# Performance work log

Measured on AMD Instinct MI355X. Metric: run time of the kernel, lower is better.

Reference implementation:

```python
import jax, jax.numpy as jnp
import numpy as np

HIDDEN = 64
NUM_HEADS = 2
HEAD_DIM = HIDDEN // NUM_HEADS  # 32


def setup_inputs() -> dict:
    key = jax.random.key(0)
    ks = jax.random.split(key, 10)
    B, L = 8, 2048
    s = 1.0 / np.sqrt(HIDDEN)
    return {
        "hidden_states": jax.random.normal(ks[0], (B, L, HIDDEN), dtype=jnp.float32),
        "qx": jax.random.normal(ks[1], (B, L, HIDDEN), dtype=jnp.float32),
        "Wq": jax.random.uniform(ks[2], (HIDDEN, HIDDEN), jnp.float32, -s, s),
        "bq": jax.random.uniform(ks[3], (HIDDEN,), jnp.float32, -s, s),
        "Wk": jax.random.uniform(ks[4], (HIDDEN, HIDDEN), jnp.float32, -s, s),
        "bk": jax.random.uniform(ks[5], (HIDDEN,), jnp.float32, -s, s),
        "Wv": jax.random.uniform(ks[6], (HIDDEN, HIDDEN), jnp.float32, -s, s),
        "bv": jax.random.uniform(ks[7], (HIDDEN,), jnp.float32, -s, s),
        "Wo": jax.random.uniform(ks[8], (HIDDEN, HIDDEN), jnp.float32, -s, s),
        "bo": jax.random.uniform(ks[9], (HIDDEN,), jnp.float32, -s, s),
    }


def _split_heads(x):
    # [B, L, HIDDEN] -> [B, H, L, HEAD_DIM]
    B, L, _ = x.shape
    return x.reshape(B, L, NUM_HEADS, HEAD_DIM).transpose(0, 2, 1, 3)


def reference(hidden_states, qx, Wq, bq, Wk, bk, Wv, bv, Wo, bo):
    # NOTE: faithful to original - query AND value come from qx, key from hidden_states.
    q = _split_heads(qx @ Wq.T + bq)              # [B, H, Lq, D]
    k = _split_heads(hidden_states @ Wk.T + bk)   # [B, H, Lk, D]
    v = _split_heads(qx @ Wv.T + bv)              # [B, H, Lq, D]
    scores = jnp.einsum("bhqd,bhkd->bhqk", q, k) / np.sqrt(HEAD_DIM).astype(np.float32)
    probs = jax.nn.softmax(scores, axis=-1)       # [B, H, Lq, Lk]
    ctx = jnp.einsum("bhqk,bhkd->bhqd", probs, v)
    B, H, L, D = ctx.shape
    ctx = ctx.transpose(0, 2, 1, 3).reshape(B, L, H * D)
    out = ctx @ Wo.T + bo
    return out, probs
```

## Files before the change

### kernel.cpp

```cpp
#include <hip/hip_runtime.h>
#include <math.h>

#define NB 8
#define SEQ 2048
#define HID 64
#define HDIM 32
#define ROWS (NB * SEQ)
#define OUT_ELEMS (ROWS * HID)
#define QSCALE 0.25503486f

typedef __attribute__((ext_vector_type(8))) short bf16x8;
typedef __attribute__((ext_vector_type(4))) float f32x4;
typedef __attribute__((ext_vector_type(4))) uint u32x4;

__device__ __forceinline__ ushort f2bf(float f) {
    uint u = __builtin_bit_cast(uint, f);
    u += 0x7FFFu + ((u >> 16) & 1u);
    return (ushort)(u >> 16);
}
__device__ __forceinline__ float bf2f(ushort h) {
    uint u = ((uint)h) << 16;
    return __builtin_bit_cast(float, u);
}
__device__ __forceinline__ uint cvt_pk_bf16(float lo, float hi) {
    uint r;
    asm("v_cvt_pk_bf16_f32 %0, %1, %2" : "=v"(r) : "v"(lo), "v"(hi));
    return r;
}
__device__ __forceinline__ void glds16(const ushort* g, ushort* l) {
    __builtin_amdgcn_global_load_lds(
        (const __attribute__((address_space(1))) uint*)(g),
        (__attribute__((address_space(3))) uint*)(l), 16, 0, 0);
}

__global__ __launch_bounds__(256, 1)
void qkv_proj_kernel(const float* __restrict__ hs, const float* __restrict__ qx,
                     const float* __restrict__ Wq, const float* __restrict__ bq,
                     const float* __restrict__ Wk, const float* __restrict__ bk,
                     const float* __restrict__ Wv, const float* __restrict__ bv,
                     ushort* __restrict__ q_hi, ushort* __restrict__ q_lo,
                     ushort* __restrict__ k_hi, ushort* __restrict__ vt_hi)
{
    __shared__ __align__(16) float xq_lds[64][64];
    __shared__ __align__(16) float xh_lds[64][64];
    __shared__ float vbuf[64][65];

    const int t  = threadIdx.x;
    const int r0 = blockIdx.x * 64;
    const int b  = r0 >> 11;

#pragma unroll
    for (int u = 0; u < 4; ++u) {
        const int idx = t + 256 * u;
        const int rr = idx >> 4, kk = (idx & 15) * 4;
        *(float4*)&xq_lds[rr][kk] = *(const float4*)(qx + (size_t)(r0 + rr) * HID + kk);
        *(float4*)&xh_lds[rr][kk] = *(const float4*)(hs + (size_t)(r0 + rr) * HID + kk);
    }
    __syncthreads();

    const int c = t & 63, w = t >> 6;
    const int rw = w * 16;
    const int h = c >> 5, d = c & 31;
    const size_t obase = ((size_t)((b * 2 + h) * SEQ) + (r0 & 2047) + rw) * 32 + d;

    {
        float4 wr[16];
#pragma unroll
        for (int i = 0; i < 16; ++i) wr[i] = *(const float4*)(Wq + c * 64 + 4 * i);
        const float bc = bq[c];
        f32x4 acc[16];
#pragma unroll
        for (int r = 0; r < 16; ++r) acc[r] = (f32x4){0.f, 0.f, 0.f, 0.f};
#pragma unroll
        for (int k4 = 0; k4 < 16; ++k4)
#pragma unroll
            for (int r = 0; r < 16; ++r) {
                const float4 x4 = *(const float4*)&xq_lds[rw + r][k4 * 4];
                acc[r][0] += x4.x * wr[k4].x; acc[r][1] += x4.y * wr[k4].y;
                acc[r][2] += x4.z * wr[k4].z; acc[r][3] += x4.w * wr[k4].w;
            }
#pragma unroll
        for (int r = 0; r < 16; ++r) {
            const float v = (acc[r][0] + acc[r][1] + acc[r][2] + acc[r][3] + bc) * QSCALE;
            const ushort hv = f2bf(v);
            q_hi[obase + (size_t)r * 32] = hv;
            q_lo[obase + (size_t)r * 32] = f2bf(v - bf2f(hv));
        }
    }
    {
        float4 wr[16];
#pragma unroll
        for (int i = 0; i < 16; ++i) wr[i] = *(const float4*)(Wk + c * 64 + 4 * i);
        const float bc = bk[c];
        f32x4 acc[16];
#pragma unroll
        for (int r = 0; r < 16; ++r) acc[r] = (f32x4){0.f, 0.f, 0.f, 0.f};
#pragma unroll
        for (int k4 = 0; k4 < 16; ++k4)
#pragma unroll
            for (int r = 0; r < 16; ++r) {
                const float4 x4 = *(const float4*)&xh_lds[rw + r][k4 * 4];
                acc[r][0] += x4.x * wr[k4].x; acc[r][1] += x4.y * wr[k4].y;
                acc[r][2] += x4.z * wr[k4].z; acc[r][3] += x4.w * wr[k4].w;
            }
#pragma unroll
        for (int r = 0; r < 16; ++r) {
            const float v = acc[r][0] + acc[r][1] + acc[r][2] + acc[r][3] + bc;
            k_hi[obase + (size_t)r * 32] = f2bf(v);
        }
    }
    {
        float4 wr[16];
#pragma unroll
        for (int i = 0; i < 16; ++i) wr[i] = *(const float4*)(Wv + c * 64 + 4 * i);
        const float bc = bv[c];
        f32x4 acc[16];
#pragma unroll
        for (int r = 0; r < 16; ++r) acc[r] = (f32x4){0.f, 0.f, 0.f, 0.f};
#pragma unroll
        for (int k4 = 0; k4 < 16; ++k4)
#pragma unroll
            for (int r = 0; r < 16; ++r) {
                const float4 x4 = *(const float4*)&xq_lds[rw + r][k4 * 4];
                acc[r][0] += x4.x * wr[k4].x; acc[r][1] += x4.y * wr[k4].y;
                acc[r][2] += x4.z * wr[k4].z; acc[r][3] += x4.w * wr[k4].w;
            }
#pragma unroll
        for (int r = 0; r < 16; ++r)
            vbuf[rw + r][c] = acc[r][0] + acc[r][1] + acc[r][2] + acc[r][3] + bc;
    }
    __syncthreads();

#pragma unroll
    for (int g = 0; g < 2; ++g) {
        const int row8 = (g * 4 + w) * 8;
        bf16x8 hi8;
#pragma unroll
        for (int e = 0; e < 8; ++e) hi8[e] = (short)f2bf(vbuf[row8 + e][c]);
        const size_t vo = ((size_t)((b * 2 + h) * 32) + d) * SEQ + (r0 & 2047) + row8;
        *reinterpret_cast<bf16x8*>(vt_hi + vo) = hi8;
    }
}

__global__ __launch_bounds__(256, 2)
void zsum_kernel(const ushort* __restrict__ q_hi, const ushort* __restrict__ q_lo,
                 const ushort* __restrict__ k_hi, float* __restrict__ rz_ws)
{
    __shared__ float z_buf[4][64];

    const int bid   = blockIdx.x;
    const int swz   = (bid & 7) * 64 + (bid >> 3);
    const int slice = swz >> 5;
    const int qb    = swz & 31;
    const int q0 = qb * 64;

    const int tid  = threadIdx.x;
    const int w    = tid >> 6, lane = tid & 63;
    const int lg   = lane >> 4, li = lane & 15;
    const int cq0  = w * 512;

    bf16x8 aqh[4], aql[4];
#pragma unroll
    for (int rt = 0; rt < 4; ++rt) {
        const size_t qoff = ((size_t)slice * SEQ + q0 + rt * 16 + li) * 32 + lg * 8;
        aqh[rt] = *(const bf16x8*)(q_hi + qoff);
        aql[rt] = *(const bf16x8*)(q_lo + qoff);
    }
    const size_t kbase = (size_t)slice * SEQ * 32;
    auto Kf = [&](int j16) {
        return *(const bf16x8*)(k_hi + kbase + (size_t)(cq0 + j16 * 16 + li) * 32 + lg * 8);
    };

    float zacc[16];
#pragma unroll
    for (int i = 0; i < 16; ++i) zacc[i] = 0.f;
    bf16x8 bh = Kf(0);
#pragma unroll 2
    for (int ct = 0; ct < 32; ++ct) {
        const bf16x8 bn = Kf(ct < 31 ? ct + 1 : 31);
#pragma unroll
        for (int rt = 0; rt < 4; ++rt) {
            f32x4 a = {0.f, 0.f, 0.f, 0.f};
            a = __builtin_amdgcn_mfma_f32_16x16x32_bf16(aqh[rt], bh, a, 0, 0, 0);
            a = __builtin_amdgcn_mfma_f32_16x16x32_bf16(aql[rt], bh, a, 0, 0, 0);
#pragma unroll
            for (int r = 0; r < 4; ++r) zacc[rt * 4 + r] += __builtin_amdgcn_exp2f(a[r]);
        }
        bh = bn;
    }
#pragma unroll
    for (int m = 1; m < 16; m <<= 1)
#pragma unroll
        for (int i = 0; i < 16; ++i) zacc[i] += __shfl_xor(zacc[i], m, 64);
    if (li == 0) {
#pragma unroll
        for (int rt = 0; rt < 4; ++rt)
#pragma unroll
            for (int r = 0; r < 4; ++r)
                z_buf[w][rt * 16 + lg * 4 + r] = zacc[rt * 4 + r];
    }
    __syncthreads();
    if (tid < 64) {
        const float z = z_buf[0][tid] + z_buf[1][tid] + z_buf[2][tid] + z_buf[3][tid];
        rz_ws[(size_t)slice * SEQ + q0 + tid] = 1.0f / z;
    }
}

__global__ __launch_bounds__(512, 4)
void attn_kernel(const ushort* __restrict__ q_hi, const ushort* __restrict__ q_lo,
                 const ushort* __restrict__ k_hi, const ushort* __restrict__ vt_hi,
                 const float* __restrict__ rz_ws, float* __restrict__ d_out)
{
    __shared__ __align__(16) ushort kbuf[3][2048];
    __shared__ __align__(16) ushort vbuf[3][2048];
    __shared__ __align__(16) float  ps[64 * 68];

    const int bid   = blockIdx.x;
    const int swz   = (bid & 7) * 64 + (bid >> 3);
    const int slice = swz >> 5;
    const int qb    = swz & 31;
    const int bb = slice >> 1, hh = slice & 1;
    const int q0 = qb * 64;

    const int tid  = threadIdx.x;
    const int wid  = tid >> 6, lane = tid & 63;
    const int lg   = lane >> 4, li = lane & 15;
    const int rt   = wid & 3;
    const int cs   = wid >> 2;

    const size_t qoff = ((size_t)slice * SEQ + q0 + rt * 16 + li) * 32 + lg * 8;
    const bf16x8 aqh = *(const bf16x8*)(q_hi + qoff);
    const bf16x8 aql = *(const bf16x8*)(q_lo + qoff);

    float rcpz[4];
#pragma unroll
    for (int r = 0; r < 4; ++r)
        rcpz[r] = rz_ws[(size_t)slice * SEQ + q0 + rt * 16 + lg * 4 + r];

    const ushort* kslice = k_hi + (size_t)slice * SEQ * 32;
    const ushort* vslice = vt_hi + (size_t)slice * 32 * SEQ;
    float* probs = d_out + OUT_ELEMS + ((size_t)slice * SEQ + q0) * SEQ;

    auto STAGE = [&](int t, int ring) {
        const int j0 = t * 64;
        if (wid < 4) {
            const int col = wid * 16 + (lane >> 2);
            const int cg  = (lane & 3) ^ ((lane >> 2) & 3);
            glds16(kslice + (size_t)(j0 + col) * 32 + cg * 8,
                   &kbuf[ring][wid * 512 + lane * 8]);
        } else {
            const int w2  = wid - 4;
            const int row = w2 * 8 + (lane >> 3);
            const int cg  = (lane & 7) ^ (row & 7);
            glds16(vslice + (size_t)row * SEQ + j0 + cg * 8,
                   &vbuf[ring][w2 * 512 + lane * 8]);
        }
    };

    STAGE(0, 0); STAGE(1, 1);

    f32x4 pacc = {0.f, 0.f, 0.f, 0.f};
    int rc = 0, rs = 2;

#pragma unroll 1
    for (int t = 0; t < 32; ++t) {
        asm volatile("s_waitcnt lgkmcnt(0)" ::: "memory");
        __builtin_amdgcn_s_barrier();
        __builtin_amdgcn_sched_barrier(0);
        if (t + 2 < 32) STAGE(t + 2, rs);
        if (t == 0)       asm volatile("s_waitcnt vmcnt(2)" ::: "memory");
        else if (t == 1)  asm volatile("s_waitcnt vmcnt(4)" ::: "memory");
        else if (t <= 29) asm volatile("s_waitcnt vmcnt(6)" ::: "memory");
        else if (t == 30) asm volatile("s_waitcnt vmcnt(5)" ::: "memory");
        else              asm volatile("s_waitcnt vmcnt(4)" ::: "memory");
        __builtin_amdgcn_s_barrier();
        __builtin_amdgcn_sched_barrier(0);

#pragma unroll
        for (int h2 = 0; h2 < 2; ++h2) {
            const int c16 = cs * 2 + h2;
            const bf16x8 bk = *(const bf16x8*)
                &kbuf[rc][(c16 * 16 + li) * 32 + ((lg ^ (li & 3)) * 8)];
            f32x4 a = {0.f, 0.f, 0.f, 0.f};
            a = __builtin_amdgcn_mfma_f32_16x16x32_bf16(aqh, bk, a, 0, 0, 0);
            a = __builtin_amdgcn_mfma_f32_16x16x32_bf16(aql, bk, a, 0, 0, 0);
#pragma unroll
            for (int r = 0; r < 4; ++r)
                ps[(rt * 16 + lg * 4 + r) * 68 + c16 * 16 + li] =
                    __builtin_amdgcn_exp2f(a[r]) * rcpz[r];
        }
        asm volatile("s_waitcnt lgkmcnt(0)" ::: "memory");
        __builtin_amdgcn_s_barrier();
        __builtin_amdgcn_sched_barrier(0);

#pragma unroll
        for (int ch = 0; ch < 2; ++ch) {
            const int pbase = (rt * 16 + li) * 68 + ch * 32 + lg * 8;
            const f32x4 pa = *(const f32x4*)&ps[pbase];
            const f32x4 pb = *(const f32x4*)&ps[pbase + 4];
            u32x4 pk;
            pk[0] = cvt_pk_bf16(pa[0], pa[1]); pk[1] = cvt_pk_bf16(pa[2], pa[3]);
            pk[2] = cvt_pk_bf16(pb[0], pb[1]); pk[3] = cvt_pk_bf16(pb[2], pb[3]);
            const bf16x8 ap = __builtin_bit_cast(bf16x8, pk);
            const int vr = cs * 16 + li;
            const bf16x8 bv = *(const bf16x8*)
                &vbuf[rc][vr * 64 + (((ch * 4 + lg) ^ (vr & 7)) * 8)];
            pacc = __builtin_amdgcn_mfma_f32_16x16x32_bf16(ap, bv, pacc, 0, 0, 0);
        }
#pragma unroll
        for (int u = 0; u < 2; ++u) {
            const int fid = tid + 512 * u;
            const int row = fid >> 4, c4 = fid & 15;
            const f32x4 pv = *(const f32x4*)&ps[row * 68 + c4 * 4];
            *(f32x4*)(probs + (size_t)row * SEQ + t * 64 + c4 * 4) = pv;
        }

        rc = (rc == 2) ? 0 : rc + 1;
        rs = (rs == 2) ? 0 : rs + 1;
    }

#pragma unroll
    for (int r = 0; r < 4; ++r)
        d_out[((size_t)bb * SEQ + q0 + rt * 16 + lg * 4 + r) * HID
              + hh * HDIM + cs * 16 + li] = pacc[r];
}

__global__ __launch_bounds__(256, 1)
void out_proj_kernel(const float* __restrict__ Wo, const float* __restrict__ bo,
                     float* __restrict__ out)
{
    const int c    = threadIdx.x & 63;
    const int rloc = threadIdx.x >> 6;

    float4 wo[16];
#pragma unroll
    for (int i = 0; i < 16; ++i) wo[i] = *(const float4*)(Wo + c * 64 + 4 * i);
    const float boc = bo[c];

    for (int rg = blockIdx.x; rg < ROWS / 4; rg += gridDim.x) {
        const int row = rg * 4 + rloc;
        const float* x = out + (size_t)row * HID;
        float a = 0.f;
#pragma unroll
        for (int i = 0; i < 16; ++i) {
            const float4 x4 = *(const float4*)(x + 4 * i);
            a += x4.x * wo[i].x + x4.y * wo[i].y + x4.z * wo[i].z + x4.w * wo[i].w;
        }
        out[(size_t)row * HID + c] = a + boc;
    }
}

extern "C" void kernel_launch(void* const* d_in, const int* in_sizes, int n_in,
                              void* d_out, int out_size, void* d_ws, size_t ws_size,
                              hipStream_t stream)
{
    const float* hs = (const float*)d_in[0];
    const float* qx = (const float*)d_in[1];
    const float* Wq = (const float*)d_in[2];
    const float* bq = (const float*)d_in[3];
    const float* Wk = (const float*)d_in[4];
    const float* bk = (const float*)d_in[5];
    const float* Wv = (const float*)d_in[6];
    const float* bv = (const float*)d_in[7];
    const float* Wo = (const float*)d_in[8];
    const float* bo = (const float*)d_in[9];
    float* out = (float*)d_out;

    const size_t N = (size_t)16 * SEQ * 32;
    ushort* q_hi  = (ushort*)d_ws;
    ushort* q_lo  = q_hi + N;
    ushort* k_hi  = q_lo + N;
    ushort* vt_hi = k_hi + N;
    float*  rz_ws = (float*)(vt_hi + N);

    qkv_proj_kernel<<<256, 256, 0, stream>>>(hs, qx, Wq, bq, Wk, bk, Wv, bv,
                                             q_hi, q_lo, k_hi, vt_hi);
    zsum_kernel<<<512, 256, 0, stream>>>(q_hi, q_lo, k_hi, rz_ws);
    attn_kernel<<<512, 512, 0, stream>>>(q_hi, q_lo, k_hi, vt_hi, rz_ws, out);
    out_proj_kernel<<<512, 256, 0, stream>>>(Wo, bo, out);
}
```

Baseline: 104.6 us.

## Give each wave its own 16-row Q tile with private score buffer

The attention block now covers 128 query rows, and each of the 8 waves owns 16 rows, computing all 64 key columns and both V halves itself. Each wave writes scores to a private LDS slice, so two block-wide barriers per iteration are dropped and the loaded K/V tiles are reused across twice as many query rows. The grid is halved to 256 blocks and the occupancy hint is lowered. In exchange, each wave does more MFMA work and needs more registers, there are fewer blocks to fill the CUs, and the pipeline wait counts were retuned by hand.

```diff
diff --git a/kernel.cpp b/kernel.cpp
--- a/kernel.cpp
+++ b/kernel.cpp
@@ -206,40 +206,39 @@
     }
 }
 
-__global__ __launch_bounds__(512, 4)
+__global__ __launch_bounds__(512, 2)
 void attn_kernel(const ushort* __restrict__ q_hi, const ushort* __restrict__ q_lo,
                  const ushort* __restrict__ k_hi, const ushort* __restrict__ vt_hi,
                  const float* __restrict__ rz_ws, float* __restrict__ d_out)
 {
     __shared__ __align__(16) ushort kbuf[3][2048];
     __shared__ __align__(16) ushort vbuf[3][2048];
-    __shared__ __align__(16) float  ps[64 * 68];
+    __shared__ __align__(16) float  ps[8][16 * 68];
 
     const int bid   = blockIdx.x;
-    const int swz   = (bid & 7) * 64 + (bid >> 3);
-    const int slice = swz >> 5;
-    const int qb    = swz & 31;
+    const int swz   = (bid & 7) * 32 + (bid >> 3);
+    const int slice = swz >> 4;
+    const int qb    = swz & 15;
     const int bb = slice >> 1, hh = slice & 1;
-    const int q0 = qb * 64;
+    const int q0 = qb * 128;
 
     const int tid  = threadIdx.x;
     const int wid  = tid >> 6, lane = tid & 63;
     const int lg   = lane >> 4, li = lane & 15;
-    const int rt   = wid & 3;
-    const int cs   = wid >> 2;
-
-    const size_t qoff = ((size_t)slice * SEQ + q0 + rt * 16 + li) * 32 + lg * 8;
+
+    const size_t qoff = ((size_t)slice * SEQ + q0 + wid * 16 + li) * 32 + lg * 8;
     const bf16x8 aqh = *(const bf16x8*)(q_hi + qoff);
     const bf16x8 aql = *(const bf16x8*)(q_lo + qoff);
 
     float rcpz[4];
 #pragma unroll
     for (int r = 0; r < 4; ++r)
-        rcpz[r] = rz_ws[(size_t)slice * SEQ + q0 + rt * 16 + lg * 4 + r];
+        rcpz[r] = rz_ws[(size_t)slice * SEQ + q0 + wid * 16 + lg * 4 + r];
 
     const ushort* kslice = k_hi + (size_t)slice * SEQ * 32;
     const ushort* vslice = vt_hi + (size_t)slice * 32 * SEQ;
-    float* probs = d_out + OUT_ELEMS + ((size_t)slice * SEQ + q0) * SEQ;
+    float* probs = d_out + OUT_ELEMS + ((size_t)slice * SEQ + q0 + wid * 16) * SEQ;
+    float* psw = &ps[wid][0];
 
     auto STAGE = [&](int t, int ring) {
         const int j0 = t * 64;
@@ -259,26 +258,21 @@
 
     STAGE(0, 0); STAGE(1, 1);
 
-    f32x4 pacc = {0.f, 0.f, 0.f, 0.f};
-    int rc = 0, rs = 2;
+    f32x4 pacc[2] = {{0.f,0.f,0.f,0.f}, {0.f,0.f,0.f,0.f}};
 
 #pragma unroll 1
     for (int t = 0; t < 32; ++t) {
-        asm volatile("s_waitcnt lgkmcnt(0)" ::: "memory");
+        const int rc = t % 3, rs = (t + 2) % 3;
+        if (t == 0)       asm volatile("s_waitcnt vmcnt(1)" ::: "memory");
+        else if (t == 1)  asm volatile("s_waitcnt vmcnt(5)" ::: "memory");
+        else if (t == 31) asm volatile("s_waitcnt vmcnt(8)" ::: "memory");
+        else              asm volatile("s_waitcnt vmcnt(9)" ::: "memory");
         __builtin_amdgcn_s_barrier();
         __builtin_amdgcn_sched_barrier(0);
         if (t + 2 < 32) STAGE(t + 2, rs);
-        if (t == 0)       asm volatile("s_waitcnt vmcnt(2)" ::: "memory");
-        else if (t == 1)  asm volatile("s_waitcnt vmcnt(4)" ::: "memory");
-        else if (t <= 29) asm volatile("s_waitcnt vmcnt(6)" ::: "memory");
-        else if (t == 30) asm volatile("s_waitcnt vmcnt(5)" ::: "memory");
-        else              asm volatile("s_waitcnt vmcnt(4)" ::: "memory");
-        __builtin_amdgcn_s_barrier();
-        __builtin_amdgcn_sched_barrier(0);
-
-#pragma unroll
-        for (int h2 = 0; h2 < 2; ++h2) {
-            const int c16 = cs * 2 + h2;
+
+#pragma unroll
+        for (int c16 = 0; c16 < 4; ++c16) {
             const bf16x8 bk = *(const bf16x8*)
                 &kbuf[rc][(c16 * 16 + li) * 32 + ((lg ^ (li & 3)) * 8)];
             f32x4 a = {0.f, 0.f, 0.f, 0.f};
@@ -286,43 +280,45 @@
             a = __builtin_amdgcn_mfma_f32_16x16x32_bf16(aql, bk, a, 0, 0, 0);
 #pragma unroll
             for (int r = 0; r < 4; ++r)
-                ps[(rt * 16 + lg * 4 + r) * 68 + c16 * 16 + li] =
+                psw[(lg * 4 + r) * 68 + c16 * 16 + li] =
                     __builtin_amdgcn_exp2f(a[r]) * rcpz[r];
         }
         asm volatile("s_waitcnt lgkmcnt(0)" ::: "memory");
-        __builtin_amdgcn_s_barrier();
         __builtin_amdgcn_sched_barrier(0);
 
 #pragma unroll
+        for (int u = 0; u < 4; ++u) {
+            const int fid = lane + 64 * u;
+            const int row = fid >> 4, c4 = fid & 15;
+            const f32x4 pv = *(const f32x4*)&psw[row * 68 + c4 * 4];
+            *(f32x4*)(probs + (size_t)row * SEQ + t * 64 + c4 * 4) = pv;
+        }
+
+#pragma unroll
         for (int ch = 0; ch < 2; ++ch) {
-            const int pbase = (rt * 16 + li) * 68 + ch * 32 + lg * 8;
-            const f32x4 pa = *(const f32x4*)&ps[pbase];
-            const f32x4 pb = *(const f32x4*)&ps[pbase + 4];
+            const int pbase = li * 68 + ch * 32 + lg * 8;
+            const f32x4 pa = *(const f32x4*)&psw[pbase];
+            const f32x4 pb = *(const f32x4*)&psw[pbase + 4];
             u32x4 pk;
             pk[0] = cvt_pk_bf16(pa[0], pa[1]); pk[1] = cvt_pk_bf16(pa[2], pa[3]);
             pk[2] = cvt_pk_bf16(pb[0], pb[1]); pk[3] = cvt_pk_bf16(pb[2], pb[3]);
             const bf16x8 ap = __builtin_bit_cast(bf16x8, pk);
-            const int vr = cs * 16 + li;
-            const bf16x8 bv = *(const bf16x8*)
-                &vbuf[rc][vr * 64 + (((ch * 4 + lg) ^ (vr & 7)) * 8)];
-            pacc = __builtin_amdgcn_mfma_f32_16x16x32_bf16(ap, bv, pacc, 0, 0, 0);
-        }
-#pragma unroll
-        for (int u = 0; u < 2; ++u) {
-            const int fid = tid + 512 * u;
-            const int row = fid >> 4, c4 = fid & 15;
-            const f32x4 pv = *(const f32x4*)&ps[row * 68 + c4 * 4];
-            *(f32x4*)(probs + (size_t)row * SEQ + t * 64 + c4 * 4) = pv;
-        }
-
-        rc = (rc == 2) ? 0 : rc + 1;
-        rs = (rs == 2) ? 0 : rs + 1;
-    }
-
-#pragma unroll
-    for (int r = 0; r < 4; ++r)
-        d_out[((size_t)bb * SEQ + q0 + rt * 16 + lg * 4 + r) * HID
-              + hh * HDIM + cs * 16 + li] = pacc[r];
+#pragma unroll
+            for (int dt = 0; dt < 2; ++dt) {
+                const int vr = dt * 16 + li;
+                const bf16x8 bv = *(const bf16x8*)
+                    &vbuf[rc][vr * 64 + (((ch * 4 + lg) ^ (vr & 7)) * 8)];
+                pacc[dt] = __builtin_amdgcn_mfma_f32_16x16x32_bf16(ap, bv, pacc[dt], 0, 0, 0);
+            }
+        }
+    }
+
+#pragma unroll
+    for (int dt = 0; dt < 2; ++dt)
+#pragma unroll
+        for (int r = 0; r < 4; ++r)
+            d_out[((size_t)bb * SEQ + q0 + wid * 16 + lg * 4 + r) * HID
+                  + hh * HDIM + dt * 16 + li] = pacc[dt][r];
 }
 
 __global__ __launch_bounds__(256, 1)
@@ -376,6 +372,6 @@
     qkv_proj_kernel<<<256, 256, 0, stream>>>(hs, qx, Wq, bq, Wk, bk, Wv, bv,
                                              q_hi, q_lo, k_hi, vt_hi);
     zsum_kernel<<<512, 256, 0, stream>>>(q_hi, q_lo, k_hi, rz_ws);
-    attn_kernel<<<512, 512, 0, stream>>>(q_hi, q_lo, k_hi, vt_hi, rz_ws, out);
+    attn_kernel<<<256, 512, 0, stream>>>(q_hi, q_lo, k_hi, vt_hi, rz_ws, out);
     out_proj_kernel<<<512, 256, 0, stream>>>(Wo, bo, out);
 }
```

After: 105.1 us. Within noise of the previous version (+0.5%).
